# Kernel optimization log

Hardware: AMD Instinct MI355X
Metric: run time of the kernel (lower is better)

The kernel has to match this reference:

```python
import jax, jax.numpy as jnp
import numpy as np

N = 12                      # total wires
LAYERS = 2
INIT_W = [0, 1, 2]
PK_W = [3, 4, 5, 6, 7]
PD_W = [8, 9, 10, 11]
KEYS = ['init_euler', 'pk_coup', 'pd_coup', 'pk_local', 'pd_local']
SHAPES = [(LAYERS, 3, 3), (LAYERS, 3, 5), (LAYERS, 3, 4), (LAYERS, 5), (LAYERS, 4)]
# Assumed physiological bounds (DEFAULT_PK_BOUNDS / DEFAULT_PD_BOUNDS not in snippet)
PK_BOUNDS = np.array([[0.1, 5.0], [1.0, 20.0], [10.0, 100.0], [0.05, 2.0], [0.1, 10.0]], dtype=np.float32)
PD_BOUNDS = np.array([[0.01, 1.0], [0.1, 5.0], [1.0, 50.0], [0.05, 2.0]], dtype=np.float32)
X_GATE = jnp.array([[0, 1], [1, 0]], dtype=jnp.complex64)


def ry(t):
    c, s = jnp.cos(t / 2), jnp.sin(t / 2)
    return jnp.stack([jnp.stack([c, -s], -1), jnp.stack([s, c], -1)], -2).astype(jnp.complex64)


def rx(t):
    c, s = jnp.cos(t / 2), jnp.sin(t / 2)
    return jnp.stack([jnp.stack([c + 0j, -1j * s], -1), jnp.stack([-1j * s, c + 0j], -1)], -2).astype(jnp.complex64)


def rz(t):
    em, ep = jnp.exp(-1j * t / 2), jnp.exp(1j * t / 2)
    z = jnp.zeros_like(em)
    return jnp.stack([jnp.stack([em, z], -1), jnp.stack([z, ep], -1)], -2).astype(jnp.complex64)


def apply_1q(state, gate, w):
    # state: (B, 2^N); gate: (2,2) shared or (B,2,2) per-sample
    B = state.shape[0]
    s = state.reshape(B, 2 ** w, 2, 2 ** (N - 1 - w))
    if gate.ndim == 3:
        s = jnp.einsum('bij,bxjy->bxiy', gate, s)
    else:
        s = jnp.einsum('ij,bxjy->bxiy', gate, s)
    return s.reshape(B, -1)


def apply_ctrl(state, gate, c, t):
    # controlled-gate: apply 2x2 `gate` on target wire t where control wire c == 1
    B = state.shape[0]
    a, b = (c, t) if c < t else (t, c)
    s = state.reshape(B, 2 ** a, 2, 2 ** (b - a - 1), 2, 2 ** (N - 1 - b))
    if c < t:
        sub = jnp.einsum('ij,bamjc->bamic', gate, s[:, :, 1])
        s = s.at[:, :, 1].set(sub)
    else:
        sub = jnp.einsum('ij,bajmc->baimc', gate, s[:, :, :, :, 1])
        s = s.at[:, :, :, :, 1].set(sub)
    return s.reshape(B, -1)


def expz(state, w):
    B = state.shape[0]
    p = (state.real ** 2 + state.imag ** 2).reshape(B, 2 ** w, 2, 2 ** (N - 1 - w))
    p = p.sum(axis=(1, 3))  # (B, 2)
    return p[:, 0] - p[:, 1]


def _unpack(theta):
    w, off = {}, 0
    for name, shape in zip(KEYS, SHAPES):
        size = int(np.prod(shape))
        w[name] = theta[off:off + size].reshape(shape)
        off += size
    return w


def _forward(covariates, dose_intensities, theta):
    inputs = jnp.concatenate([covariates, dose_intensities[:, None]], axis=1).astype(jnp.float32)  # (B, 3)
    B = inputs.shape[0]
    state = jnp.zeros((B, 2 ** N), jnp.complex64).at[:, 0].set(1.0)
    # input encoding: per-sample RY angles on init wires
    for i, w in enumerate(INIT_W):
        state = apply_1q(state, ry(inputs[:, i]), w)
    wd = _unpack(theta)
    for l in range(LAYERS):
        for q in range(3):
            e = wd['init_euler'][l, q]
            state = apply_1q(state, rx(e[0]), INIT_W[q])
            state = apply_1q(state, ry(e[1]), INIT_W[q])
            state = apply_1q(state, rz(e[2]), INIT_W[q])
        state = apply_ctrl(state, X_GATE, INIT_W[0], INIT_W[1])
        state = apply_ctrl(state, X_GATE, INIT_W[1], INIT_W[2])
        state = apply_ctrl(state, X_GATE, INIT_W[2], INIT_W[0])
        for i in range(3):
            for j in range(5):
                state = apply_ctrl(state, ry(wd['pk_coup'][l, i, j]), INIT_W[i], PK_W[j])
        for j in range(5):
            state = apply_1q(state, ry(wd['pk_local'][l, j]), PK_W[j])
        for i in range(3):
            for k in range(4):
                state = apply_ctrl(state, ry(wd['pd_coup'][l, i, k]), INIT_W[i], PD_W[k])
        for k in range(4):
            state = apply_1q(state, ry(wd['pd_local'][l, k]), PD_W[k])
    raw = jnp.stack([expz(state, w) for w in PK_W + PD_W], axis=1)  # (B, 9)
    s = 0.5 * (raw + 1.0)
    pk = PK_BOUNDS[:, 0] + s[:, :5] * (PK_BOUNDS[:, 1] - PK_BOUNDS[:, 0])
    pd = PD_BOUNDS[:, 0] + s[:, 5:] * (PD_BOUNDS[:, 1] - PD_BOUNDS[:, 0])
    return pk, pd


def setup_inputs() -> dict:
    key = jax.random.key(0)
    k1, k2, k3, k4 = jax.random.split(key, 4)
    B = 512
    return {
        'subject_ids': jax.random.randint(k1, (B,), 0, B),
        'covariates': jax.random.normal(k2, (B, 2), dtype=jnp.float32),
        'dose_intensities': jax.random.uniform(k3, (B,), dtype=jnp.float32),
        'theta': jax.random.normal(k4, (90,), dtype=jnp.float32) * 0.1,
    }


def reference(subject_ids, covariates, dose_intensities, theta):
    return _forward(covariates, dose_intensities, theta)
```

## Files before the change

### kernel.cpp

```cpp
#include <hip/hip_runtime.h>
#include <math.h>

__global__ __launch_bounds__(256)
void qpkpd_fused_kernel(const float* __restrict__ cov,
                        const float* __restrict__ dose,
                        const float* __restrict__ theta,
                        float* __restrict__ out, int B)
{
    __shared__ float sEr[24], sEi[24];
    __shared__ float sA0[72];
    __shared__ float sCA1[72], sSA1[72];
    __shared__ float sV0r[64], sV0i[64];
    __shared__ float sV1r[64], sV1i[64];
    __shared__ float sGr[576], sGi[576];
    __shared__ float sMr[576], sMi[576];
    __shared__ float sS[576];
    __shared__ float4 sT4[63];
    float* sTf = (float*)sT4;

    const int t = threadIdx.x;

    if (t < 6) {
        int l = t / 3, q = t % 3;
        float e0 = 0.5f*theta[l*9 + q*3 + 0];
        float e1 = 0.5f*theta[l*9 + q*3 + 1];
        float e2 = 0.5f*theta[l*9 + q*3 + 2];
        float s0 = __sinf(e0), c0 = __cosf(e0);
        float s1 = __sinf(e1), c1 = __cosf(e1);
        float s2 = __sinf(e2), c2 = __cosf(e2);
        float m00r =  c1*c0, m00i =  s1*s0;
        float m01r = -s1*c0, m01i = -c1*s0;
        float m10r =  s1*c0, m10i = -c1*s0;
        float m11r =  c1*c0, m11i = -s1*s0;
        int base = t*4;
        sEr[base+0] = c2*m00r + s2*m00i;  sEi[base+0] = c2*m00i - s2*m00r;
        sEr[base+1] = c2*m01r + s2*m01i;  sEi[base+1] = c2*m01i - s2*m01r;
        sEr[base+2] = c2*m10r - s2*m10i;  sEi[base+2] = c2*m10i + s2*m10r;
        sEr[base+3] = c2*m11r - s2*m11i;  sEi[base+3] = c2*m11i + s2*m11r;
    }
    if (t < 72) {
        int w = t >> 3, c = t & 7;
        float b0 = (float)((c>>2)&1), b1 = (float)((c>>1)&1), b2 = (float)(c&1);
        float a0, a1;
        if (w < 5) {
            a0 = theta[72 + w] + b0*theta[18 + w] + b1*theta[23 + w] + b2*theta[28 + w];
            a1 = theta[77 + w] + b0*theta[33 + w] + b1*theta[38 + w] + b2*theta[43 + w];
        } else {
            int k = w - 5;
            a0 = theta[82 + k] + b0*theta[48 + k] + b1*theta[52 + k] + b2*theta[56 + k];
            a1 = theta[86 + k] + b0*theta[60 + k] + b1*theta[64 + k] + b2*theta[68 + k];
        }
        sA0[t] = a0;
        sCA1[t] = __cosf(a1);
        sSA1[t] = __sinf(a1);
    }
    __syncthreads();

    if (t < 64) {
        int r = t >> 3, c = t & 7;
        int rb0=(r>>2)&1, rb1=(r>>1)&1, rb2=r&1;
        int cb0=(c>>2)&1, cb1=(c>>1)&1, cb2=c&1;
        int nb1 = rb1 ^ rb0;
        int nb2 = rb2 ^ nb1;
        int nb0 = rb0 ^ nb2;
        int pr = (nb0<<2)|(nb1<<1)|nb2;
        #pragma unroll
        for (int l = 0; l < 2; ++l) {
            int i0 = (l*3+0)*4 + rb0*2 + cb0;
            int i1 = (l*3+1)*4 + rb1*2 + cb1;
            int i2 = (l*3+2)*4 + rb2*2 + cb2;
            float xr = sEr[i0], xi = sEi[i0];
            float yr = sEr[i1], yi = sEi[i1];
            float zr = xr*yr - xi*yi, zi = xr*yi + xi*yr;
            float wr = sEr[i2], wi = sEi[i2];
            float tr = zr*wr - zi*wi, ti = zr*wi + zi*wr;
            if (l == 0) { sV0r[pr*8+c] = tr; sV0i[pr*8+c] = ti; }
            else        { sV1r[pr*8+c] = tr; sV1i[pr*8+c] = ti; }
        }
    }
    __syncthreads();

    if (t < 64) {
        int c1 = t >> 3, c2 = t & 7;
        float cd[9], sh[9];
        #pragma unroll
        for (int v = 0; v < 9; ++v) {
            float av = sA0[v*8+c1], bv = sA0[v*8+c2];
            cd[v] = __cosf(0.5f*(av-bv));
            sh[v] = 0.5f*(av+bv);
        }
        float P[9], Q[9];
        #pragma unroll
        for (int w = 0; w < 9; ++w) {
            float C = 1.0f;
            #pragma unroll
            for (int v = 0; v < 9; ++v) if (v != w) C *= cd[v];
            P[w] = C*__cosf(sh[w]);
            Q[w] = C*__sinf(sh[w]);
        }
        float pr[8], pi[8];
        #pragma unroll
        for (int cp = 0; cp < 8; ++cp) {
            float r1 = sV1r[cp*8+c1], i1 = sV1i[cp*8+c1];
            float r2 = sV1r[cp*8+c2], i2 = sV1i[cp*8+c2];
            pr[cp] = r1*r2 + i1*i2;
            pi[cp] = i1*r2 - r1*i2;
        }
        #pragma unroll
        for (int w = 0; w < 9; ++w) {
            float Kr=0.f, Ki=0.f, Lr=0.f, Li=0.f;
            #pragma unroll
            for (int cp = 0; cp < 8; ++cp) {
                float cw = sCA1[w*8+cp], sw = sSA1[w*8+cp];
                Kr += cw*pr[cp]; Ki += cw*pi[cp];
                Lr += sw*pr[cp]; Li += sw*pi[cp];
            }
            sGr[w*64 + t] = P[w]*Kr - Q[w]*Lr;
            sGi[w*64 + t] = P[w]*Ki - Q[w]*Li;
        }
    }
    __syncthreads();

    for (int idx = t; idx < 576; idx += 256) {
        int w = idx >> 6, rc = idx & 63;
        int k1 = rc >> 3, c = rc & 7;
        float mr = 0.f, mi = 0.f;
        #pragma unroll
        for (int k2 = 0; k2 < 8; ++k2) {
            float wr = sGr[w*64 + k1*8 + k2], wi = sGi[w*64 + k1*8 + k2];
            float vr = sV0r[k2*8 + c],        vi = sV0i[k2*8 + c];
            mr += wr*vr + wi*vi;
            mi += wi*vr - wr*vi;
        }
        sMr[idx] = mr; sMi[idx] = mi;
    }
    __syncthreads();

    for (int idx = t; idx < 576; idx += 256) {
        int w = idx >> 6, rc = idx & 63;
        int r = rc >> 3, c = rc & 7;
        float s = 0.f;
        #pragma unroll
        for (int k = 0; k < 8; ++k)
            s += sV0r[k*8 + r]*sMr[w*64 + k*8 + c] - sV0i[k*8 + r]*sMi[w*64 + k*8 + c];
        sS[idx] = s;
    }
    __syncthreads();

    if (t < 243) {
        const float sc[9] = {2.45f, 9.5f, 45.0f, 0.975f, 4.95f,
                             0.495f, 2.45f, 24.5f, 0.975f};
        int w = t / 27, rem = t % 27;
        int j = rem / 9, k = (rem / 3) % 3, l = rem % 3;
        float s = 0.f;
        #pragma unroll
        for (int aj = 0; aj < 2; ++aj) {
            bool vj = (j == 1) || (aj == 0);
            int a0b = (j == 2) || (j == 1 && aj == 1);
            int b0b = (j == 2) || (j == 1 && aj == 0);
            #pragma unroll
            for (int ak = 0; ak < 2; ++ak) {
                bool vk = (k == 1) || (ak == 0);
                int a1b = (k == 2) || (k == 1 && ak == 1);
                int b1b = (k == 2) || (k == 1 && ak == 0);
                #pragma unroll
                for (int al = 0; al < 2; ++al) {
                    bool vl = (l == 1) || (al == 0);
                    int a2b = (l == 2) || (l == 1 && al == 1);
                    int b2b = (l == 2) || (l == 1 && al == 0);
                    if (vj && vk && vl) {
                        int r = a0b*4 + a1b*2 + a2b;
                        int c = b0b*4 + b1b*2 + b2b;
                        s += sS[w*64 + r*8 + c];
                    }
                }
            }
        }
        sTf[w*28 + rem] = s * sc[w];
    }
    if (t < 9) sTf[t*28 + 27] = 0.f;
    __syncthreads();

    int b = blockIdx.x*256 + t;
    if (b >= B) return;

    float2 xy = ((const float2*)cov)[b];
    float x2 = dose[b];
    float h0 = 0.5f*xy.x, h1 = 0.5f*xy.y, h2 = 0.5f*x2;
    float s0 = __sinf(h0), c0 = __cosf(h0);
    float s1 = __sinf(h1), c1 = __cosf(h1);
    float s2 = __sinf(h2), c2 = __cosf(h2);

    float q0[3] = {c0*c0, c0*s0, s0*s0};
    float q1[3] = {c1*c1, c1*s1, s1*s1};
    float q2[3] = {c2*c2, c2*s2, s2*s2};

    float4 m4[7];
    float* m = (float*)m4;
    #pragma unroll
    for (int j = 0; j < 3; ++j) {
        #pragma unroll
        for (int k = 0; k < 3; ++k) {
            float r = q0[j]*q1[k];
            #pragma unroll
            for (int l = 0; l < 3; ++l)
                m[j*9 + k*3 + l] = r*q2[l];
        }
    }
    m[27] = 0.f;

    const float off[9] = {2.55f, 10.5f, 55.0f, 1.025f, 5.05f,
                          0.505f, 2.55f, 25.5f, 1.025f};
    #pragma unroll
    for (int w = 0; w < 9; ++w) {
        float g = off[w];
        #pragma unroll
        for (int i = 0; i < 7; ++i) {
            float4 tt = sT4[w*7 + i];
            float4 mm = m4[i];
            g += tt.x*mm.x + tt.y*mm.y + tt.z*mm.z + tt.w*mm.w;
        }
        if (w < 5) out[b*5 + w] = g;
        else       out[B*5 + b*4 + (w-5)] = g;
    }
}

extern "C" void kernel_launch(void* const* d_in, const int* in_sizes, int n_in,
                              void* d_out, int out_size, void* d_ws, size_t ws_size,
                              hipStream_t stream)
{
    const float* cov   = (const float*)d_in[1];
    const float* dose  = (const float*)d_in[2];
    const float* theta = (const float*)d_in[3];
    float* out = (float*)d_out;
    const int B = in_sizes[2];

    int grid = (B + 255) / 256;
    qpkpd_fused_kernel<<<grid, 256, 0, stream>>>(cov, dose, theta, out, B);
}
```

Baseline: 11.08 us.

## Widen block to 576 threads and parallelise theta-only precompute across all threads

The block grows to 576 threads and the grid is hard-coded to 8 blocks of 64 samples each, so every thread takes part in the theta-dependent matrix build. Work that 64 threads did serially per element (cos-difference products, P/Q factors, the per-w G accumulation) is now spread with one element per thread. Per-sample input loads and trig are moved to the start so they overlap the precompute. Several shared arrays become interleaved float2 with transposed V0/M so the inner products use float4 reads. Because the grid no longer depends on B, the kernel only covers up to 512 samples.

```diff
diff --git a/kernel.cpp b/kernel.cpp
--- a/kernel.cpp
+++ b/kernel.cpp
@@ -1,45 +1,73 @@
 #include <hip/hip_runtime.h>
 #include <math.h>
 
-__global__ __launch_bounds__(256)
-void qpkpd_fused_kernel(const float* __restrict__ cov,
-                        const float* __restrict__ dose,
-                        const float* __restrict__ theta,
-                        float* __restrict__ out, int B)
+#define NT 576
+
+__global__ __launch_bounds__(NT)
+void qpkpd_kernel(const float* __restrict__ cov,
+                  const float* __restrict__ dose,
+                  const float* __restrict__ theta,
+                  float* __restrict__ out, int B)
 {
-    __shared__ float sEr[24], sEi[24];
-    __shared__ float sA0[72];
-    __shared__ float sCA1[72], sSA1[72];
-    __shared__ float sV0r[64], sV0i[64];
-    __shared__ float sV1r[64], sV1i[64];
-    __shared__ float sGr[576], sGi[576];
-    __shared__ float sMr[576], sMi[576];
-    __shared__ float sS[576];
-    __shared__ float4 sT4[63];
-    float* sTf = (float*)sT4;
+    __shared__ float  sA0[72];
+    __shared__ float2 sCS1[72];
+    __shared__ float  sV1r[64], sV1i[64];
+    __shared__ float2 sV0T[64];
+    __shared__ float  sCD[576];
+    __shared__ float2 sP2[512];
+    __shared__ float2 sG2[576];
+    __shared__ float2 sMT[576];
+    __shared__ float  sS[576];
+    __shared__ float  sTf[252];
 
     const int t = threadIdx.x;
 
-    if (t < 6) {
-        int l = t / 3, q = t % 3;
-        float e0 = 0.5f*theta[l*9 + q*3 + 0];
-        float e1 = 0.5f*theta[l*9 + q*3 + 1];
-        float e2 = 0.5f*theta[l*9 + q*3 + 2];
-        float s0 = __sinf(e0), c0 = __cosf(e0);
-        float s1 = __sinf(e1), c1 = __cosf(e1);
-        float s2 = __sinf(e2), c2 = __cosf(e2);
-        float m00r =  c1*c0, m00i =  s1*s0;
-        float m01r = -s1*c0, m01i = -c1*s0;
-        float m10r =  s1*c0, m10i = -c1*s0;
-        float m11r =  c1*c0, m11i = -s1*s0;
-        int base = t*4;
-        sEr[base+0] = c2*m00r + s2*m00i;  sEi[base+0] = c2*m00i - s2*m00r;
-        sEr[base+1] = c2*m01r + s2*m01i;  sEi[base+1] = c2*m01i - s2*m01r;
-        sEr[base+2] = c2*m10r - s2*m10i;  sEi[base+2] = c2*m10i + s2*m10r;
-        sEr[base+3] = c2*m11r - s2*m11i;  sEi[base+3] = c2*m11i + s2*m11r;
-    }
-    if (t < 72) {
-        int w = t >> 3, c = t & 7;
+    float q0[3], q1[3], q2[3];
+    int bS = 0;
+    if (t >= 512) {
+        bS = blockIdx.x * 64 + (t - 512);
+        float2 xy = ((const float2*)cov)[bS];
+        float xd = dose[bS];
+        float h0 = 0.5f*xy.x, h1 = 0.5f*xy.y, h2 = 0.5f*xd;
+        float s0=__sinf(h0), c0=__cosf(h0);
+        float s1=__sinf(h1), c1=__cosf(h1);
+        float s2=__sinf(h2), c2=__cosf(h2);
+        q0[0]=c0*c0; q0[1]=c0*s0; q0[2]=s0*s0;
+        q1[0]=c1*c1; q1[1]=c1*s1; q1[2]=s1*s1;
+        q2[0]=c2*c2; q2[1]=c2*s2; q2[2]=s2*s2;
+    }
+
+    if (t < 128) {
+        int l = t >> 6, rc = t & 63;
+        int r = rc >> 3, c = rc & 7;
+        float tr = 1.f, ti = 0.f;
+        #pragma unroll
+        for (int q = 0; q < 3; ++q) {
+            float h0 = 0.5f*theta[l*9 + q*3 + 0];
+            float h1 = 0.5f*theta[l*9 + q*3 + 1];
+            float h2 = 0.5f*theta[l*9 + q*3 + 2];
+            float s0=__sinf(h0), c0=__cosf(h0);
+            float s1=__sinf(h1), c1=__cosf(h1);
+            float s2=__sinf(h2), c2=__cosf(h2);
+            int a = (r >> (2-q)) & 1, bb = (c >> (2-q)) & 1;
+            float rab  = (a==bb) ? c1 : (a ? s1 : -s1);
+            float ra1b = (a!=bb) ? c1 : (a ? s1 : -s1);
+            float mr = rab*c0, mi = -ra1b*s0;
+            float sa = a ? -1.f : 1.f;
+            float er = mr*c2 + sa*mi*s2;
+            float ei = mi*c2 - sa*mr*s2;
+            float nr = tr*er - ti*ei;
+            ti = tr*ei + ti*er;
+            tr = nr;
+        }
+        int rb0=(r>>2)&1, rb1=(r>>1)&1, rb2=r&1;
+        int nb1 = rb1 ^ rb0, nb2 = rb2 ^ nb1, nb0 = rb0 ^ nb2;
+        int pr = (nb0<<2)|(nb1<<1)|nb2;
+        if (l == 0) sV0T[c*8 + pr] = make_float2(tr, ti);
+        else { sV1r[pr*8 + c] = tr; sV1i[pr*8 + c] = ti; }
+    } else if (t < 200) {
+        int idx = t - 128;
+        int w = idx >> 3, c = idx & 7;
         float b0 = (float)((c>>2)&1), b1 = (float)((c>>1)&1), b2 = (float)(c&1);
         float a0, a1;
         if (w < 5) {
@@ -50,100 +78,78 @@
             a0 = theta[82 + k] + b0*theta[48 + k] + b1*theta[52 + k] + b2*theta[56 + k];
             a1 = theta[86 + k] + b0*theta[60 + k] + b1*theta[64 + k] + b2*theta[68 + k];
         }
-        sA0[t] = a0;
-        sCA1[t] = __cosf(a1);
-        sSA1[t] = __sinf(a1);
-    }
-    __syncthreads();
-
-    if (t < 64) {
-        int r = t >> 3, c = t & 7;
-        int rb0=(r>>2)&1, rb1=(r>>1)&1, rb2=r&1;
-        int cb0=(c>>2)&1, cb1=(c>>1)&1, cb2=c&1;
-        int nb1 = rb1 ^ rb0;
-        int nb2 = rb2 ^ nb1;
-        int nb0 = rb0 ^ nb2;
-        int pr = (nb0<<2)|(nb1<<1)|nb2;
-        #pragma unroll
-        for (int l = 0; l < 2; ++l) {
-            int i0 = (l*3+0)*4 + rb0*2 + cb0;
-            int i1 = (l*3+1)*4 + rb1*2 + cb1;
-            int i2 = (l*3+2)*4 + rb2*2 + cb2;
-            float xr = sEr[i0], xi = sEi[i0];
-            float yr = sEr[i1], yi = sEi[i1];
-            float zr = xr*yr - xi*yi, zi = xr*yi + xi*yr;
-            float wr = sEr[i2], wi = sEi[i2];
-            float tr = zr*wr - zi*wi, ti = zr*wi + zi*wr;
-            if (l == 0) { sV0r[pr*8+c] = tr; sV0i[pr*8+c] = ti; }
-            else        { sV1r[pr*8+c] = tr; sV1i[pr*8+c] = ti; }
-        }
-    }
-    __syncthreads();
-
-    if (t < 64) {
-        int c1 = t >> 3, c2 = t & 7;
-        float cd[9], sh[9];
+        sA0[idx] = a0;
+        sCS1[idx] = make_float2(__cosf(a1), __sinf(a1));
+    }
+    __syncthreads();
+
+    {
+        int v = t >> 6, p = t & 63;
+        sCD[t] = __cosf(0.5f*(sA0[v*8 + (p>>3)] - sA0[v*8 + (p&7)]));
+    }
+    if (t < 512) {
+        int cp = t >> 6, p = t & 63;
+        int c1 = p >> 3, c2 = p & 7;
+        float r1 = sV1r[cp*8+c1], i1 = sV1i[cp*8+c1];
+        float r2 = sV1r[cp*8+c2], i2 = sV1i[cp*8+c2];
+        sP2[t] = make_float2(r1*r2 + i1*i2, i1*r2 - r1*i2);
+    }
+    __syncthreads();
+
+    {
+        int w = t >> 6, p = t & 63;
+        int c1 = p >> 3, c2 = p & 7;
+        float sh = 0.5f*(sA0[w*8+c1] + sA0[w*8+c2]);
+        float ssh = __sinf(sh), csh = __cosf(sh);
+        float C = 1.f;
         #pragma unroll
         for (int v = 0; v < 9; ++v) {
-            float av = sA0[v*8+c1], bv = sA0[v*8+c2];
-            cd[v] = __cosf(0.5f*(av-bv));
-            sh[v] = 0.5f*(av+bv);
-        }
-        float P[9], Q[9];
-        #pragma unroll
-        for (int w = 0; w < 9; ++w) {
-            float C = 1.0f;
-            #pragma unroll
-            for (int v = 0; v < 9; ++v) if (v != w) C *= cd[v];
-            P[w] = C*__cosf(sh[w]);
-            Q[w] = C*__sinf(sh[w]);
-        }
-        float pr[8], pi[8];
+            float f = sCD[v*64 + p];
+            C *= (v == w) ? 1.f : f;
+        }
+        float P = C*csh, Q = C*ssh;
+        const float4* cs4 = (const float4*)(&sCS1[w*8]);
+        float4 csa = cs4[0], csb = cs4[1], csc = cs4[2], csd = cs4[3];
+        float cw[8] = {csa.x,csa.z,csb.x,csb.z,csc.x,csc.z,csd.x,csd.z};
+        float sw[8] = {csa.y,csa.w,csb.y,csb.w,csc.y,csc.w,csd.y,csd.w};
+        float Kr=0.f, Ki=0.f, Lr=0.f, Li=0.f;
         #pragma unroll
         for (int cp = 0; cp < 8; ++cp) {
-            float r1 = sV1r[cp*8+c1], i1 = sV1i[cp*8+c1];
-            float r2 = sV1r[cp*8+c2], i2 = sV1i[cp*8+c2];
-            pr[cp] = r1*r2 + i1*i2;
-            pi[cp] = i1*r2 - r1*i2;
-        }
-        #pragma unroll
-        for (int w = 0; w < 9; ++w) {
-            float Kr=0.f, Ki=0.f, Lr=0.f, Li=0.f;
-            #pragma unroll
-            for (int cp = 0; cp < 8; ++cp) {
-                float cw = sCA1[w*8+cp], sw = sSA1[w*8+cp];
-                Kr += cw*pr[cp]; Ki += cw*pi[cp];
-                Lr += sw*pr[cp]; Li += sw*pi[cp];
-            }
-            sGr[w*64 + t] = P[w]*Kr - Q[w]*Lr;
-            sGi[w*64 + t] = P[w]*Ki - Q[w]*Li;
-        }
-    }
-    __syncthreads();
-
-    for (int idx = t; idx < 576; idx += 256) {
-        int w = idx >> 6, rc = idx & 63;
-        int k1 = rc >> 3, c = rc & 7;
+            float2 pp = sP2[cp*64 + p];
+            Kr += cw[cp]*pp.x; Ki += cw[cp]*pp.y;
+            Lr += sw[cp]*pp.x; Li += sw[cp]*pp.y;
+        }
+        sG2[t] = make_float2(P*Kr - Q*Lr, P*Ki - Q*Li);
+    }
+    __syncthreads();
+
+    {
+        int w = t >> 6, rc = t & 63, k1 = rc >> 3, c = rc & 7;
+        const float4* gp = (const float4*)(&sG2[w*64 + k1*8]);
+        const float4* vp = (const float4*)(&sV0T[c*8]);
         float mr = 0.f, mi = 0.f;
         #pragma unroll
-        for (int k2 = 0; k2 < 8; ++k2) {
-            float wr = sGr[w*64 + k1*8 + k2], wi = sGi[w*64 + k1*8 + k2];
-            float vr = sV0r[k2*8 + c],        vi = sV0i[k2*8 + c];
-            mr += wr*vr + wi*vi;
-            mi += wi*vr - wr*vi;
-        }
-        sMr[idx] = mr; sMi[idx] = mi;
-    }
-    __syncthreads();
-
-    for (int idx = t; idx < 576; idx += 256) {
-        int w = idx >> 6, rc = idx & 63;
-        int r = rc >> 3, c = rc & 7;
+        for (int i = 0; i < 4; ++i) {
+            float4 g = gp[i];
+            float4 v = vp[i];
+            mr += g.x*v.x + g.y*v.y + g.z*v.z + g.w*v.w;
+            mi += g.y*v.x - g.x*v.y + g.w*v.z - g.z*v.w;
+        }
+        sMT[w*64 + c*8 + k1] = make_float2(mr, mi);
+    }
+    __syncthreads();
+
+    {
+        int w = t >> 6, rc = t & 63, r = rc >> 3, c = rc & 7;
+        const float4* vp = (const float4*)(&sV0T[r*8]);
+        const float4* mp = (const float4*)(&sMT[w*64 + c*8]);
         float s = 0.f;
         #pragma unroll
-        for (int k = 0; k < 8; ++k)
-            s += sV0r[k*8 + r]*sMr[w*64 + k*8 + c] - sV0i[k*8 + r]*sMi[w*64 + k*8 + c];
-        sS[idx] = s;
+        for (int i = 0; i < 4; ++i) {
+            float4 v = vp[i], m = mp[i];
+            s += v.x*m.x - v.y*m.y + v.z*m.z - v.w*m.w;
+        }
+        sS[w*64 + r*8 + c] = s;
     }
     __syncthreads();
 
@@ -178,50 +184,38 @@
         }
         sTf[w*28 + rem] = s * sc[w];
     }
-    if (t < 9) sTf[t*28 + 27] = 0.f;
-    __syncthreads();
-
-    int b = blockIdx.x*256 + t;
-    if (b >= B) return;
-
-    float2 xy = ((const float2*)cov)[b];
-    float x2 = dose[b];
-    float h0 = 0.5f*xy.x, h1 = 0.5f*xy.y, h2 = 0.5f*x2;
-    float s0 = __sinf(h0), c0 = __cosf(h0);
-    float s1 = __sinf(h1), c1 = __cosf(h1);
-    float s2 = __sinf(h2), c2 = __cosf(h2);
-
-    float q0[3] = {c0*c0, c0*s0, s0*s0};
-    float q1[3] = {c1*c1, c1*s1, s1*s1};
-    float q2[3] = {c2*c2, c2*s2, s2*s2};
-
-    float4 m4[7];
-    float* m = (float*)m4;
-    #pragma unroll
-    for (int j = 0; j < 3; ++j) {
-        #pragma unroll
-        for (int k = 0; k < 3; ++k) {
-            float r = q0[j]*q1[k];
+    if (t >= 256 && t < 265) sTf[(t-256)*28 + 27] = 0.f;
+    __syncthreads();
+
+    if (t >= 512 && bS < B) {
+        float4 m4[7];
+        float* m = (float*)m4;
+        #pragma unroll
+        for (int j = 0; j < 3; ++j) {
             #pragma unroll
-            for (int l = 0; l < 3; ++l)
-                m[j*9 + k*3 + l] = r*q2[l];
-        }
-    }
-    m[27] = 0.f;
-
-    const float off[9] = {2.55f, 10.5f, 55.0f, 1.025f, 5.05f,
-                          0.505f, 2.55f, 25.5f, 1.025f};
-    #pragma unroll
-    for (int w = 0; w < 9; ++w) {
-        float g = off[w];
-        #pragma unroll
-        for (int i = 0; i < 7; ++i) {
-            float4 tt = sT4[w*7 + i];
-            float4 mm = m4[i];
-            g += tt.x*mm.x + tt.y*mm.y + tt.z*mm.z + tt.w*mm.w;
-        }
-        if (w < 5) out[b*5 + w] = g;
-        else       out[B*5 + b*4 + (w-5)] = g;
+            for (int k = 0; k < 3; ++k) {
+                float r = q0[j]*q1[k];
+                #pragma unroll
+                for (int l = 0; l < 3; ++l)
+                    m[j*9 + k*3 + l] = r*q2[l];
+            }
+        }
+        m[27] = 0.f;
+        const float off[9] = {2.55f, 10.5f, 55.0f, 1.025f, 5.05f,
+                              0.505f, 2.55f, 25.5f, 1.025f};
+        #pragma unroll
+        for (int w = 0; w < 9; ++w) {
+            float g = off[w];
+            const float4* tp = (const float4*)(&sTf[w*28]);
+            #pragma unroll
+            for (int i = 0; i < 7; ++i) {
+                float4 tt = tp[i];
+                float4 mm = m4[i];
+                g += tt.x*mm.x + tt.y*mm.y + tt.z*mm.z + tt.w*mm.w;
+            }
+            if (w < 5) out[bS*5 + w] = g;
+            else       out[B*5 + bS*4 + (w-5)] = g;
+        }
     }
 }
 
@@ -235,6 +229,5 @@
     float* out = (float*)d_out;
     const int B = in_sizes[2];
 
-    int grid = (B + 255) / 256;
-    qpkpd_fused_kernel<<<grid, 256, 0, stream>>>(cov, dose, theta, out, B);
+    qpkpd_kernel<<<8, NT, 0, stream>>>(cov, dose, theta, out, B);
 }
```

New measurement: 10.43 us. -5.9%, faster.
